# Performance work log

Hardware: AMD Instinct MI355X
Metric: run time of the kernel (lower is better)

Reference implementation:

```python
import jax, jax.numpy as jnp
import numpy as np

NUM_NODES = 4096


def _dense_adjs(edge_index, edge_values, n):
    # edge_index: [J, 2, E] int, edge_values: [J, E] float -> [J, n, n]
    # scatter-add == torch_sparse.coalesce (duplicate edges are summed)
    def one(ei, ev):
        return jnp.zeros((n, n), ev.dtype).at[ei[0], ei[1]].add(ev)
    return jax.vmap(one)(edge_index, edge_values)


def setup_inputs() -> dict:
    key = jax.random.key(0)
    k1, k2, k3, k4 = jax.random.split(key, 4)
    J, E, C, N = 5, 150000, 2, NUM_NODES
    edge_index = jax.random.randint(k1, (J, 2, E), 0, N)
    edge_values = jax.random.uniform(k2, (J, E), dtype=jnp.float32)
    w1 = jax.random.normal(k3, (C, J), dtype=jnp.float32) * 0.01
    w2 = jax.random.normal(k4, (C, J), dtype=jnp.float32) * 0.01
    return {"edge_index": edge_index, "edge_values": edge_values, "w1": w1, "w2": w2}


def reference(edge_index, edge_values, w1, w2):
    n = NUM_NODES
    # GTConv: softmax over edge types, weighted sum of per-type adjacencies
    D = _dense_adjs(edge_index, edge_values, n)          # [J, n, n]
    f1 = jax.nn.softmax(w1, axis=1)                      # [C, J]
    f2 = jax.nn.softmax(w2, axis=1)                      # [C, J]
    A1 = jnp.einsum('cj,jmn->cmn', f1, D)                # conv1 output per channel
    A2 = jnp.einsum('cj,jmn->cmn', f2, D)                # conv2 output per channel
    # spspmm per channel == dense matmul of the (zero-padded) sparse matrices
    H = jnp.einsum('cmk,ckn->cmn', A1, A2)               # [C, n, n]
    return (H, f1, f2)
```

## Files before the change

kernel.cpp:

```cpp
#include <hip/hip_runtime.h>
#include <hip/hip_bf16.h>
#include <stdint.h>

#define JT 5
#define NE 150000
#define NC 2
#define NDIM 4096
#define KDIM 4096
#define NNZ (JT * NE)
constexpr size_t MAT = (size_t)NDIM * NDIM;
constexpr size_t HN  = (size_t)NC * MAT;

typedef __bf16 bf16x8 __attribute__((ext_vector_type(8)));
typedef float  f32x4  __attribute__((ext_vector_type(4)));

__global__ void softmax_k(const float* __restrict__ w1, const float* __restrict__ w2,
                          float* __restrict__ fbuf, float* __restrict__ out_tail) {
    int t = threadIdx.x;
    if (t < 2 * NC) {
        const float* w = (t < NC) ? w1 : w2;
        int c = t % NC;
        float v[JT];
        float mx = -1e30f;
        for (int j = 0; j < JT; ++j) { v[j] = w[c * JT + j]; mx = fmaxf(mx, v[j]); }
        float s = 0.f;
        for (int j = 0; j < JT; ++j) { v[j] = expf(v[j] - mx); s += v[j]; }
        float inv = 1.0f / s;
        for (int j = 0; j < JT; ++j) {
            float f = v[j] * inv;
            fbuf[t * JT + j] = f;
            out_tail[t * JT + j] = f;
        }
    }
}

__device__ __forceinline__ void pkadd(__bf16* base, size_t cell, float x) {
    uint16_t h = __builtin_bit_cast(uint16_t, (__bf16)x);
    uint32_t pk = (cell & 1) ? ((uint32_t)h << 16) : (uint32_t)h;
    __bf16* p = base + (cell & ~(size_t)1);
    asm volatile("global_atomic_pk_add_bf16 %0, %1, off"
                 :: "v"((uint64_t)(uintptr_t)p), "v"(pk) : "memory");
}

__global__ void scatter_pk_k(const int* __restrict__ ei, const float* __restrict__ ev,
                             const float* __restrict__ fbuf,
                             __bf16* __restrict__ A1, __bf16* __restrict__ A2) {
    int idx = blockIdx.x * blockDim.x + threadIdx.x;
    if (idx >= NNZ) return;
    int j = idx / NE;
    int e = idx - j * NE;
    int r = ei[(size_t)j * 2 * NE + e];
    int c = ei[(size_t)j * 2 * NE + NE + e];
    float v = ev[idx];
    float f10 = fbuf[j]          * v;
    float f11 = fbuf[JT + j]     * v;
    float f20 = fbuf[2 * JT + j] * v;
    float f21 = fbuf[3 * JT + j] * v;
    size_t rc = (size_t)r * NDIM + c;
    size_t cr = (size_t)c * NDIM + r;
    pkadd(A1,       rc, f10);
    pkadd(A1 + MAT, rc, f11);
    pkadd(A2,       cr, f20);
    pkadd(A2 + MAT, cr, f21);
}

#define BM 256
#define BN 256
#define BK 64
#define NT (KDIM / BK)
#define TILE_E (BM * BK)

__device__ __forceinline__ void gl_lds16(const __bf16* g, __bf16* l) {
    __builtin_amdgcn_global_load_lds(
        (const __attribute__((address_space(1))) void*)(uintptr_t)g,
        (__attribute__((address_space(3))) void*)l, 16, 0, 0);
}

#define PHASE(MH, KS, READB, ...) do {                                            \
    _Pragma("unroll")                                                             \
    for (int i = 0; i < 4; ++i)                                                   \
        af[i] = *(const bf16x8*)(ldsAc +                                          \
            ((((rA + ((MH)*4 + i) * 16) * 128) + (KS)*64 + kb) ^ swz));           \
    if (READB) {                                                                  \
        _Pragma("unroll")                                                         \
        for (int n = 0; n < 4; ++n)                                               \
            bfr[n] = *(const bf16x8*)(ldsBc +                                     \
                ((((rB + n * 16) * 128) + (KS)*64 + kb) ^ swz));                  \
    }                                                                             \
    __VA_ARGS__;                                                                  \
    __builtin_amdgcn_s_barrier();                                                 \
    asm volatile("s_waitcnt lgkmcnt(0)" ::: "memory");                            \
    __builtin_amdgcn_s_setprio(1);                                                \
    _Pragma("unroll")                                                             \
    for (int i = 0; i < 4; ++i)                                                   \
        _Pragma("unroll")                                                         \
        for (int n = 0; n < 4; ++n)                                               \
            acc[(MH)*4 + i][n] = __builtin_amdgcn_mfma_f32_16x16x32_bf16(         \
                af[i], bfr[n], acc[(MH)*4 + i][n], 0, 0, 0);                      \
    __builtin_amdgcn_s_setprio(0);                                                \
    __builtin_amdgcn_s_barrier();                                                 \
} while (0)

__global__ __launch_bounds__(512, 2) void gemm_k(const __bf16* __restrict__ A,
                                                 const __bf16* __restrict__ B,
                                                 float* __restrict__ C) {
    __shared__ __align__(16) __bf16 sm[4 * TILE_E];

    const int u    = threadIdx.x;
    const int lane = u & 63;
    const int wv   = u >> 6;
    const int wm   = wv >> 2;
    const int wn   = wv & 3;
    const size_t matoff = (size_t)blockIdx.z * MAT;
    const size_t brow   = (size_t)blockIdx.y * BM;
    const size_t bcol   = (size_t)blockIdx.x * BN;

    const int srow = u >> 3;
    const int kc   = (u & 7) ^ (srow & 7);
    const __bf16* Abase = A + matoff + (brow + srow) * KDIM + kc * 8;
    const __bf16* Bbase = B + matoff + (bcol + srow) * KDIM + kc * 8;

    char* const smb = (char*)sm;
    auto issueA = [&](int unit, int tt) {
        const __bf16* src = Abase + (size_t)unit * 64 * KDIM + (size_t)tt * BK;
        __bf16* dst = (__bf16*)(smb + (tt & 1) * 65536 + unit * 8192 + wv * 1024);
        gl_lds16(src, dst);
    };
    auto issueB = [&](int unit, int tt) {
        const __bf16* src = Bbase + (size_t)unit * 64 * KDIM + (size_t)tt * BK;
        __bf16* dst = (__bf16*)(smb + (tt & 1) * 65536 + 32768 + unit * 8192 + wv * 1024);
        gl_lds16(src, dst);
    };

    const int rA  = wm * 128 + (lane & 15);
    const int rB  = wn * 64  + (lane & 15);
    const int kb  = (lane >> 4) * 16;
    const int swz = (lane & 7) << 4;

    f32x4 acc[8][4];
#pragma unroll
    for (int m = 0; m < 8; ++m)
#pragma unroll
        for (int n = 0; n < 4; ++n) acc[m][n] = (f32x4){0.f, 0.f, 0.f, 0.f};

    bf16x8 af[4], bfr[4];

#pragma unroll
    for (int i = 0; i < 4; ++i) issueA(i, 0);
#pragma unroll
    for (int i = 0; i < 4; ++i) issueB(i, 0);

    for (int t = 0; t < NT; ++t) {
        const char* ldsAc = smb + (t & 1) * 65536;
        const char* ldsBc = ldsAc + 32768;
        const int nxt = t + 1;
        const bool hasNext = nxt < NT;

        if (hasNext) {
            issueA(0, nxt); issueA(1, nxt);
            asm volatile("s_waitcnt vmcnt(2)" ::: "memory");
        } else {
            asm volatile("s_waitcnt vmcnt(0)" ::: "memory");
        }
        __builtin_amdgcn_s_barrier();
        asm volatile("" ::: "memory");

        PHASE(0, 0, true,  if (hasNext) { issueA(2, nxt); issueA(3, nxt);
                                          issueB(0, nxt); issueB(1, nxt); });
        PHASE(1, 0, false, if (hasNext) { issueB(2, nxt); issueB(3, nxt); });
        PHASE(0, 1, true,  );
        PHASE(1, 1, false, );
    }

    float* Cc = C + matoff;
#pragma unroll
    for (int m = 0; m < 8; ++m) {
        int orow0 = (int)brow + wm * 128 + m * 16 + (lane >> 4) * 4;
#pragma unroll
        for (int n = 0; n < 4; ++n) {
            int ocol = (int)bcol + wn * 64 + n * 16 + (lane & 15);
            float* p = Cc + (size_t)orow0 * NDIM + ocol;
#pragma unroll
            for (int jj = 0; jj < 4; ++jj) p[(size_t)jj * NDIM] = acc[m][n][jj];
        }
    }
}

extern "C" void kernel_launch(void* const* d_in, const int* in_sizes, int n_in,
                              void* d_out, int out_size, void* d_ws, size_t ws_size,
                              hipStream_t stream) {
    const int*   ei = (const int*)d_in[0];
    const float* ev = (const float*)d_in[1];
    const float* w1 = (const float*)d_in[2];
    const float* w2 = (const float*)d_in[3];
    float* out = (float*)d_out;

    char* ws = (char*)d_ws;
    __bf16* A1b  = (__bf16*)ws;
    __bf16* A2b  = (__bf16*)(ws + HN * sizeof(__bf16));
    float*  fbuf = (float*)(ws + 2 * HN * sizeof(__bf16));
    size_t needed = 2 * HN * sizeof(__bf16) + 32 * sizeof(float);
    if (ws_size < needed) return;

    softmax_k<<<dim3(1), dim3(64), 0, stream>>>(w1, w2, fbuf, out + HN);

    hipMemsetAsync(A1b, 0, 2 * HN * sizeof(__bf16), stream);

    const int nb = (NNZ + 255) / 256;
    scatter_pk_k<<<dim3(nb), dim3(256), 0, stream>>>(ei, ev, fbuf, A1b, A2b);

    gemm_k<<<dim3(NDIM / BN, NDIM / BM, NC), dim3(512), 0, stream>>>(A1b, A2b, out);
}
```

Baseline: 387.6 us.

## Scatter into interleaved buffer with paired atomics, then repack via LDS transpose

The scatter now writes all four channel/conv values for an edge into one interleaved 8-byte cell in the output buffer, using two packed bf16 atomics instead of four scattered ones. The old version touched two distant rows and columns per edge. A new repack kernel reads the interleaved buffer through shared memory and writes the A1 and transposed A2 bf16 matrices that the GEMM expects. This is meant to cut atomic count and improve locality, at the cost of an extra full-matrix read/write pass. The output buffer is reused as scratch before the GEMM overwrites it.

```diff
diff --git a/kernel.cpp b/kernel.cpp
--- a/kernel.cpp
+++ b/kernel.cpp
@@ -34,17 +34,16 @@
     }
 }
 
-__device__ __forceinline__ void pkadd(__bf16* base, size_t cell, float x) {
-    uint16_t h = __builtin_bit_cast(uint16_t, (__bf16)x);
-    uint32_t pk = (cell & 1) ? ((uint32_t)h << 16) : (uint32_t)h;
-    __bf16* p = base + (cell & ~(size_t)1);
+__device__ __forceinline__ void pkadd2(__bf16* p, float lo, float hi) {
+    uint16_t a = __builtin_bit_cast(uint16_t, (__bf16)lo);
+    uint16_t b = __builtin_bit_cast(uint16_t, (__bf16)hi);
+    uint32_t pk = ((uint32_t)b << 16) | a;
     asm volatile("global_atomic_pk_add_bf16 %0, %1, off"
                  :: "v"((uint64_t)(uintptr_t)p), "v"(pk) : "memory");
 }
 
-__global__ void scatter_pk_k(const int* __restrict__ ei, const float* __restrict__ ev,
-                             const float* __restrict__ fbuf,
-                             __bf16* __restrict__ A1, __bf16* __restrict__ A2) {
+__global__ void scatter2_k(const int* __restrict__ ei, const float* __restrict__ ev,
+                           const float* __restrict__ fbuf, __bf16* __restrict__ Xi) {
     int idx = blockIdx.x * blockDim.x + threadIdx.x;
     if (idx >= NNZ) return;
     int j = idx / NE;
@@ -52,16 +51,49 @@
     int r = ei[(size_t)j * 2 * NE + e];
     int c = ei[(size_t)j * 2 * NE + NE + e];
     float v = ev[idx];
-    float f10 = fbuf[j]          * v;
-    float f11 = fbuf[JT + j]     * v;
-    float f20 = fbuf[2 * JT + j] * v;
-    float f21 = fbuf[3 * JT + j] * v;
-    size_t rc = (size_t)r * NDIM + c;
-    size_t cr = (size_t)c * NDIM + r;
-    pkadd(A1,       rc, f10);
-    pkadd(A1 + MAT, rc, f11);
-    pkadd(A2,       cr, f20);
-    pkadd(A2 + MAT, cr, f21);
+    size_t cell = ((size_t)r * NDIM + c) * 4;
+    pkadd2(Xi + cell,     fbuf[j]          * v, fbuf[JT + j]     * v);
+    pkadd2(Xi + cell + 2, fbuf[2 * JT + j] * v, fbuf[3 * JT + j] * v);
+}
+
+__device__ __forceinline__ uint4 gather8(const ushort (*s)[65], int rr, int e8) {
+    uint4 v;
+    v.x = (uint32_t)s[rr][e8 + 0] | ((uint32_t)s[rr][e8 + 1] << 16);
+    v.y = (uint32_t)s[rr][e8 + 2] | ((uint32_t)s[rr][e8 + 3] << 16);
+    v.z = (uint32_t)s[rr][e8 + 4] | ((uint32_t)s[rr][e8 + 5] << 16);
+    v.w = (uint32_t)s[rr][e8 + 6] | ((uint32_t)s[rr][e8 + 7] << 16);
+    return v;
+}
+
+__global__ __launch_bounds__(256) void repack_k(const ushort4* __restrict__ Xi,
+                                                __bf16* __restrict__ A1,
+                                                __bf16* __restrict__ A2T) {
+    __shared__ ushort s10[64][65];
+    __shared__ ushort s11[64][65];
+    __shared__ ushort s20[64][65];
+    __shared__ ushort s21[64][65];
+    const int r0 = blockIdx.y * 64, c0 = blockIdx.x * 64;
+    const int t = threadIdx.x;
+
+#pragma unroll
+    for (int it = 0; it < 16; ++it) {
+        int li = t + 256 * it;
+        int rr = li >> 6, cc = li & 63;
+        ushort4 v = Xi[(size_t)(r0 + rr) * NDIM + (c0 + cc)];
+        s10[rr][cc] = v.x; s11[rr][cc] = v.y;
+        s20[cc][rr] = v.z; s21[cc][rr] = v.w;
+    }
+    __syncthreads();
+
+#pragma unroll
+    for (int a = 0; a < 2; ++a) {
+        int w = t + 256 * a;
+        int rr = w >> 3, e8 = (w & 7) << 3;
+        *(uint4*)(A1 +        (size_t)(r0 + rr) * NDIM + c0 + e8) = gather8(s10, rr, e8);
+        *(uint4*)(A1 + MAT +  (size_t)(r0 + rr) * NDIM + c0 + e8) = gather8(s11, rr, e8);
+        *(uint4*)(A2T +       (size_t)(c0 + rr) * NDIM + r0 + e8) = gather8(s20, rr, e8);
+        *(uint4*)(A2T + MAT + (size_t)(c0 + rr) * NDIM + r0 + e8) = gather8(s21, rr, e8);
+    }
 }
 
 #define BM 256
@@ -202,12 +234,16 @@
     size_t needed = 2 * HN * sizeof(__bf16) + 32 * sizeof(float);
     if (ws_size < needed) return;
 
+    __bf16* Xi = (__bf16*)d_out;
+
     softmax_k<<<dim3(1), dim3(64), 0, stream>>>(w1, w2, fbuf, out + HN);
 
-    hipMemsetAsync(A1b, 0, 2 * HN * sizeof(__bf16), stream);
+    hipMemsetAsync(Xi, 0, HN * sizeof(float), stream);
 
     const int nb = (NNZ + 255) / 256;
-    scatter_pk_k<<<dim3(nb), dim3(256), 0, stream>>>(ei, ev, fbuf, A1b, A2b);
+    scatter2_k<<<dim3(nb), dim3(256), 0, stream>>>(ei, ev, fbuf, Xi);
+
+    repack_k<<<dim3(64, 64), dim3(256), 0, stream>>>((const ushort4*)Xi, A1b, A2b);
 
     gemm_k<<<dim3(NDIM / BN, NDIM / BM, NC), dim3(512), 0, stream>>>(A1b, A2b, out);
 }
```

Result: faster. 358.0 us (-7.6%).
